# Optimization experiments

Hardware: AMD Instinct MI355X
Metric: run time of the kernel (lower is better)

Reference implementation:

```python
import jax, jax.numpy as jnp
import numpy as np

KH, KW = 3, 3
PAD = (1, 1, 1, 1)  # torch F.pad order: (W_left, W_right, H_top, H_bottom)
STRIDE = 1
B, CIN, COUT, H, W = 4, 32, 32, 128, 128


def setup_inputs() -> dict:
    key = jax.random.key(0)
    k1, k2, k3, k4 = jax.random.split(key, 4)
    f = jax.random.normal(k1, (B, CIN, H, W), jnp.float32)
    # orientation field components (cos/sin of a random angle field)
    theta = jax.random.uniform(k2, (B, CIN, H, W), jnp.float32, 0.0, 2.0 * np.pi)
    r0 = jnp.cos(theta)
    r1 = jnp.sin(theta)
    # learned conv weight (nn.Conv2d default uniform init, no bias)
    fan_in = CIN * KH * KW
    bound = 1.0 / np.sqrt(fan_in)
    w = jax.random.uniform(k3, (COUT, CIN, KH, KW), jnp.float32, -bound, bound)
    # frozen wr: (randn * pi * 100) / a with a = 100  ->  randn * pi
    wr = jax.random.normal(k4, (COUT, CIN, KH, KW), jnp.float32) * np.pi
    return {"f": f, "r0": r0, "r1": r1, "w": w, "wr": wr}


def _rot90(w):
    # torch: w.permute(0,1,2,4,3).flip([4]) on the (kh,kw) dims
    return jnp.flip(jnp.swapaxes(w, -1, -2), -1)


def _conv_single(f, r0, r1, w, wr):
    # f, r0, r1: (B, Cin, Hp, Wp);  w, wr: (Cout, Cin, KH, KW)
    Hp, Wp = f.shape[2], f.shape[3]
    he = Hp - PAD[0] - PAD[1]
    we = Wp - PAD[2] - PAD[3]
    s = STRIDE
    out = None
    for i in range(KH):
        for j in range(KW):
            fw = f[:, :, i:i + he:s, j:j + we:s]    # (B, Cin, h, w)
            r0w = r0[:, :, i:i + he:s, j:j + we:s]
            r1w = r1[:, :, i:i + he:s, j:j + we:s]
            c = jnp.cos(wr[:, :, i, j])[None, :, :, None, None]   # (1, Cout, Cin, 1, 1)
            sn = jnp.sin(wr[:, :, i, j])[None, :, :, None, None]
            # lambda_theta: relu of orientation-projected field, (B, Cout, Cin, h, w)
            lam = jax.nn.relu(c * r0w[:, None] + sn * r1w[:, None])
            term = jnp.einsum('bchw,oc,bochw->bohw', fw, w[:, :, i, j], lam)
            out = term if out is None else out + term
    return out  # (B, Cout, h, w)


def _forward(f, r0, r1, w, wr):
    pl, pr, pt, pb = PAD
    pad = ((0, 0), (0, 0), (pt, pb), (pl, pr))
    fp = jnp.pad(f, pad)
    r0p = jnp.pad(r0, pad)
    r1p = jnp.pad(r1, pad)
    orient = jnp.arange(4, dtype=f.dtype) * jnp.asarray(np.pi / 2, f.dtype)
    outs = []
    wk = w
    for o in range(4):
        if o > 0:
            wk = _rot90(wk)
        outs.append(_conv_single(fp, r0p, r1p, wk, wr + orient[o]))
    stacked = jnp.stack(outs, axis=2)              # (B, Cout, 4, h, w)
    idx = jnp.argmax(stacked, axis=2)              # (B, Cout, h, w)
    out = jnp.take_along_axis(stacked, idx[:, :, None], axis=2)[:, :, 0]
    out_r = orient[idx]                            # winning orientation angle
    return out, jnp.cos(out_r), jnp.sin(out_r)


def reference(f, r0, r1, w, wr):
    return _forward(f, r0, r1, w, wr)
```

## Files before the change

kernel.cpp:

```cpp
#include <hip/hip_runtime.h>


typedef float v2f __attribute__((ext_vector_type(2)));

#define B_    4
#define CIN_  32
#define COUT_ 32
#define H_    128
#define W_    128
#define HW_   (H_ * W_)
#define OUTSZ_ (B_ * COUT_ * H_ * W_)

__global__ __launch_bounds__(256)
void build_wtab(const float* __restrict__ w, const float* __restrict__ wr,
                float* __restrict__ tab)
{
    int idx = blockIdx.x * 256 + threadIdx.x;
    if (idx >= CIN_ * 9 * COUT_) return;
    int oc  = idx & 31;
    int t2  = idx >> 5;
    int tap = t2 % 9;
    int cc  = t2 / 9;
    int i = tap / 3, j = tap - i * 3;
    int base = (oc * CIN_ + cc) * 9;
    float w0 = w[base + i * 3 + j];
    float w1 = w[base + (2 - j) * 3 + i];
    float w2 = w[base + (2 - i) * 3 + (2 - j)];
    float w3 = w[base + j * 3 + (2 - i)];
    float S, C;
    sincosf(wr[base + i * 3 + j], &S, &C);
    float* dst = tab + (size_t)idx * 8;
    dst[0] = C;  dst[1] = S;
    dst[2] = w0; dst[3] = w1;
    dst[4] = w2; dst[5] = w3;
    dst[6] = 0.0f; dst[7] = 0.0f;
}

#define NC_    8
#define NG_    (CIN_ / NC_)
#define ROWF_  68
#define CLSTR_ (3 * ROWF_)
#define USED_  (NC_ * CLSTR_)
#define PLANE_ 1636
#define NBUF_  (3 * PLANE_)

struct WRow { float4 a0, a1, a2; float2 b0, b1, b2; };

#define LOAD_WROW(Wd) do {                                                  \
    const float* _wp = wanchor + soff;                                      \
    (Wd).a0 = *reinterpret_cast<const float4*>(_wp - 256);                  \
    (Wd).b0 = *reinterpret_cast<const float2*>(_wp - 252);                  \
    (Wd).a1 = *reinterpret_cast<const float4*>(_wp);                        \
    (Wd).b1 = *reinterpret_cast<const float2*>(_wp + 4);                    \
    (Wd).a2 = *reinterpret_cast<const float4*>(_wp + 256);                  \
    (Wd).b2 = *reinterpret_cast<const float2*>(_wp + 260);                  \
    soff += 768;                                                            \
    soff = (soff < 72960) ? soff : 72960;    \
    __builtin_amdgcn_sched_group_barrier(0x020, 6, 0);    \
} while (0)

#define CORE_TAP(W4, W2, JJ) do {                                           \
    v2f _C2  = {(W4).x, (W4).x};                                            \
    v2f _S2  = {(W4).y, (W4).y};                                            \
    v2f _w0  = {(W4).z, (W4).z};                                            \
    v2f _w1  = {(W4).w, (W4).w};                                            \
    v2f _w2  = {(W2).x, (W2).x};                                            \
    v2f _w3  = {(W2).y, (W2).y};                                            \
    _Pragma("unroll")                                                       \
    for (int _q = 0; _q < 2; ++_q) {                                        \
        v2f _f  = _fP[_q + (JJ)];                                           \
        v2f _r0 = _aP[_q + (JJ)];                                           \
        v2f _r1 = _bP[_q + (JJ)];                                           \
        v2f _m1 = _S2 * _r1;                                                \
        v2f _u  = __builtin_elementwise_fma(_C2, _r0, _m1);                 \
        v2f _m2 = _S2 * _r0;                                                \
        v2f _vv = __builtin_elementwise_fma(_C2, _r1, -_m2);                \
        v2f _g0 = __builtin_elementwise_max(_u,  (v2f)(0.0f));              \
        v2f _g1 = __builtin_elementwise_max(_vv, (v2f)(0.0f));              \
        v2f _t0 = _f * _g0;                                                 \
        v2f _t1 = _f * _g1;                                                 \
        v2f _t2 = __builtin_elementwise_fma(_f, -_u,  _t0);                 \
        v2f _t3 = __builtin_elementwise_fma(_f, -_vv, _t1);                 \
        acc[_q][0] = __builtin_elementwise_fma(_t0, _w0, acc[_q][0]);       \
        acc[_q][1] = __builtin_elementwise_fma(_t1, _w1, acc[_q][1]);       \
        acc[_q][2] = __builtin_elementwise_fma(_t2, _w2, acc[_q][2]);       \
        acc[_q][3] = __builtin_elementwise_fma(_t3, _w3, acc[_q][3]);       \
    }                                                                       \
} while (0)

#define COMPUTE_ROW(Wr, RB, CL, II) do {                                    \
    const float* _rb = (RB);                                                \
    const int _bi = (CL) * CLSTR_ + (II) * ROWF_ + (p << 1);                \
    float4 _fA = *reinterpret_cast<const float4*>(&_rb[_bi]);               \
    float4 _fB = *reinterpret_cast<const float4*>(&_rb[_bi + 4]);           \
    float4 _aA = *reinterpret_cast<const float4*>(&_rb[PLANE_ + _bi]);      \
    float4 _aB = *reinterpret_cast<const float4*>(&_rb[PLANE_ + _bi + 4]);  \
    float4 _bA = *reinterpret_cast<const float4*>(&_rb[2 * PLANE_ + _bi]);  \
    float4 _bB = *reinterpret_cast<const float4*>(&_rb[2 * PLANE_ + _bi + 4]);\
    v2f _fP[4] = {{_fA.x,_fA.y},{_fA.z,_fA.w},{_fB.x,_fB.y},{_fB.z,_fB.w}}; \
    v2f _aP[4] = {{_aA.x,_aA.y},{_aA.z,_aA.w},{_aB.x,_aB.y},{_aB.z,_aB.w}}; \
    v2f _bP[4] = {{_bA.x,_bA.y},{_bA.z,_bA.w},{_bB.x,_bB.y},{_bB.z,_bB.w}}; \
    CORE_TAP((Wr).a0, (Wr).b0, 0);                                          \
    CORE_TAP((Wr).a1, (Wr).b1, 1);                                          \
    CORE_TAP((Wr).a2, (Wr).b2, 2);                                          \
} while (0)

#define STEP(WLD, WUSE, RB, CL, II) do {                                    \
    LOAD_WROW(WLD);                                                         \
    COMPUTE_ROW(WUSE, RB, CL, II);                                          \
} while (0)

#define STAGE_LOAD(GI) do {                                                 \
    const int _gb = chanBase + (GI) * (NC_ * HW_);                          \
    const float* _fb = f  + _gb;                                            \
    const float* _ab = r0 + _gb;                                            \
    const float* _bb = r1 + _gb;                                            \
    _Pragma("unroll")                                                       \
    for (int _k = 0; _k < 3; ++_k) {                                        \
        tF[_k] = _fb[goff[_k]]; tA[_k] = _ab[goff[_k]]; tB[_k] = _bb[goff[_k]]; \
    }                                                                       \
    if (have3) { tF[3] = _fb[goff[3]]; tA[3] = _ab[goff[3]]; tB[3] = _bb[goff[3]]; } \
} while (0)

#define STAGE_WRITE(DST) do {                                               \
    float* _d = (DST);                                                      \
    _Pragma("unroll")                                                       \
    for (int _k = 0; _k < 3; ++_k) {                                        \
        _d[             sidx[_k]] = __uint_as_float(__float_as_uint(tF[_k]) & msk[_k]); \
        _d[PLANE_     + sidx[_k]] = __uint_as_float(__float_as_uint(tA[_k]) & msk[_k]); \
        _d[2 * PLANE_ + sidx[_k]] = __uint_as_float(__float_as_uint(tB[_k]) & msk[_k]); \
    }                                                                       \
    if (have3) {                                                            \
        _d[             sidx[3]] = __uint_as_float(__float_as_uint(tF[3]) & msk[3]); \
        _d[PLANE_     + sidx[3]] = __uint_as_float(__float_as_uint(tA[3]) & msk[3]); \
        _d[2 * PLANE_ + sidx[3]] = __uint_as_float(__float_as_uint(tB[3]) & msk[3]); \
    }                                                                       \
} while (0)

__global__ __launch_bounds__(512, 3)
void orient_conv_kernel(const float* __restrict__ f,
                        const float* __restrict__ r0,
                        const float* __restrict__ r1,
                        const float* __restrict__ tab,
                        float* __restrict__ out)
{
    __shared__ float sm[2 * NBUF_];

    const int tid   = threadIdx.x;
    const int oc    = tid & 31;
    const int pxg   = tid >> 5;
    const int p     = pxg << 1;
    const int obid  = blockIdx.x;
    const int bid   = (obid & 7) * ((B_ * H_ * 2) >> 3) + (obid >> 3);
    const int b     = bid >> 8;
    const int rem   = bid & 255;
    const int h     = rem >> 1;
    const int wbase = (rem & 1) << 6;

    int      goff[4], sidx[4];
    unsigned msk[4];
#pragma unroll
    for (int k = 0; k < 4; ++k) {
        int s = tid + (k << 9);
        if (s < USED_) {
            int cl  = s / CLSTR_;
            int r2  = s - cl * CLSTR_;
            int row = r2 / ROWF_;
            int q2  = r2 - row * ROWF_;
            int col = (q2 >> 1) + ((q2 & 1) << 5);
            int gh = h + row - 1;
            int gw = wbase + col - 1;
            bool ok = ((unsigned)gh < (unsigned)H_) & ((unsigned)gw < (unsigned)W_);
            goff[k] = ok ? (cl * HW_ + gh * W_ + gw) : 0;
            msk[k]  = ok ? 0xFFFFFFFFu : 0u;
            sidx[k] = s;
        } else { goff[k] = 0; msk[k] = 0u; sidx[k] = USED_; }
    }
    const bool have3 = (tid + 1536) < USED_;
    const int chanBase = b * (CIN_ * HW_);

    v2f acc[2][4];
#pragma unroll
    for (int q = 0; q < 2; ++q)
#pragma unroll
        for (int o = 0; o < 4; ++o) acc[q][o] = (v2f)(0.0f);

    const float* wanchor = tab + (size_t)((1 << 5) | oc) * 8;
    int soff = 0;
    WRow WA, WB;
    LOAD_WROW(WA);

    float tF[4], tA[4], tB[4];
    STAGE_LOAD(0);
    STAGE_WRITE(sm);
    STAGE_LOAD(1);
    __syncthreads();

#pragma unroll 1
    for (int g = 0; g < NG_; ++g) {
        const float* rb = sm + (g & 1) * NBUF_;

#pragma unroll 1
        for (int cl = 0; cl < NC_; cl += 2) {
            STEP(WB, WA, rb, cl,     0);
            STEP(WA, WB, rb, cl,     1);
            STEP(WB, WA, rb, cl,     2);
            STEP(WA, WB, rb, cl + 1, 0);
            STEP(WB, WA, rb, cl + 1, 1);
            STEP(WA, WB, rb, cl + 1, 2);
        }

        if (g + 1 < NG_) {
            float* wbuf = sm + ((g + 1) & 1) * NBUF_;
            STAGE_WRITE(wbuf);
            if (g + 2 < NG_) STAGE_LOAD(g + 2);
            __syncthreads();
        }
    }

    const float cosv[4] = {1.0f, -4.37113883e-08f, -1.0f, 1.19248806e-08f};
    const float sinv[4] = {0.0f, 1.0f, -8.74227766e-08f, -1.0f};
#pragma unroll
    for (int q = 0; q < 2; ++q) {
#pragma unroll
        for (int k = 0; k < 2; ++k) {
            int wcol = wbase + p + q + (k << 5);
            float a0 = acc[q][0][k], a1 = acc[q][1][k];
            float a2 = acc[q][2][k], a3 = acc[q][3][k];
            float best = a0; int bi = 0;
            if (a1 > best) { best = a1; bi = 1; }
            if (a2 > best) { best = a2; bi = 2; }
            if (a3 > best) { best = a3; bi = 3; }
            size_t o = ((size_t)(b * COUT_ + oc) * H_ + h) * W_ + wcol;
            out[o]              = best;
            out[o + OUTSZ_]     = cosv[bi];
            out[o + 2 * OUTSZ_] = sinv[bi];
        }
    }
}

extern "C" void kernel_launch(void* const* d_in, const int* in_sizes, int n_in,
                              void* d_out, int out_size, void* d_ws, size_t ws_size,
                              hipStream_t stream)
{
    const float* f  = (const float*)d_in[0];
    const float* r0 = (const float*)d_in[1];
    const float* r1 = (const float*)d_in[2];
    const float* w  = (const float*)d_in[3];
    const float* wr = (const float*)d_in[4];
    float* out = (float*)d_out;
    float* tab = (float*)d_ws;

    build_wtab<<<dim3(36), dim3(256), 0, stream>>>(w, wr, tab);
    orient_conv_kernel<<<dim3(B_ * H_ * 2), dim3(512), 0, stream>>>(
        f, r0, r1, tab, out);
}
```

Baseline: 267.7 us.

## Stage inputs via global_load_lds and software-pipeline LDS row reads

Replaces the register-staged global-to-LDS copy with direct global_load_lds async loads issued at the start of each channel group, then zeroes out-of-bounds halo entries in a fixup pass after waiting on vmcnt. It also double-buffers LDS row reads into registers (RA/RB) so the next row's ds_reads overlap the current row's math, and raises the occupancy hint in launch bounds from 3 to 4 blocks. The plane stride is changed so the wave-based LDS destination layout fits. This is meant to cut register pressure and staging latency, but it depends on the lane-to-address mapping of global_load_lds matching the thread-indexed layout, and the out-of-bounds lanes still issue loads from offset 0 that the fixup must overwrite.

```diff
diff --git a/kernel.cpp b/kernel.cpp
--- a/kernel.cpp
+++ b/kernel.cpp
@@ -41,10 +41,11 @@
 #define ROWF_  68
 #define CLSTR_ (3 * ROWF_)
 #define USED_  (NC_ * CLSTR_)
-#define PLANE_ 1636
+#define PLANE_ 1668
 #define NBUF_  (3 * PLANE_)
 
 struct WRow { float4 a0, a1, a2; float2 b0, b1, b2; };
+struct RRow { float4 f0, f1, a0, a1, b0, b1; };
 
 #define LOAD_WROW(Wd) do {                                                  \
     const float* _wp = wanchor + soff;                                      \
@@ -57,6 +58,17 @@
     soff += 768;                                                            \
     soff = (soff < 72960) ? soff : 72960;    \
     __builtin_amdgcn_sched_group_barrier(0x020, 6, 0);    \
+} while (0)
+
+#define RLOAD(Rd, RB_, CL, II) do {                                         \
+    const float* _rp = (RB_) + (CL) * CLSTR_ + (II) * ROWF_ + (p << 1);     \
+    (Rd).f0 = *reinterpret_cast<const float4*>(_rp);                        \
+    (Rd).f1 = *reinterpret_cast<const float4*>(_rp + 4);                    \
+    (Rd).a0 = *reinterpret_cast<const float4*>(_rp + PLANE_);               \
+    (Rd).a1 = *reinterpret_cast<const float4*>(_rp + PLANE_ + 4);           \
+    (Rd).b0 = *reinterpret_cast<const float4*>(_rp + 2 * PLANE_);           \
+    (Rd).b1 = *reinterpret_cast<const float4*>(_rp + 2 * PLANE_ + 4);       \
+    __builtin_amdgcn_sched_group_barrier(0x100, 6, 0);      \
 } while (0)
 
 #define CORE_TAP(W4, W2, JJ) do {                                           \
@@ -88,56 +100,67 @@
     }                                                                       \
 } while (0)
 
-#define COMPUTE_ROW(Wr, RB, CL, II) do {                                    \
-    const float* _rb = (RB);                                                \
-    const int _bi = (CL) * CLSTR_ + (II) * ROWF_ + (p << 1);                \
-    float4 _fA = *reinterpret_cast<const float4*>(&_rb[_bi]);               \
-    float4 _fB = *reinterpret_cast<const float4*>(&_rb[_bi + 4]);           \
-    float4 _aA = *reinterpret_cast<const float4*>(&_rb[PLANE_ + _bi]);      \
-    float4 _aB = *reinterpret_cast<const float4*>(&_rb[PLANE_ + _bi + 4]);  \
-    float4 _bA = *reinterpret_cast<const float4*>(&_rb[2 * PLANE_ + _bi]);  \
-    float4 _bB = *reinterpret_cast<const float4*>(&_rb[2 * PLANE_ + _bi + 4]);\
-    v2f _fP[4] = {{_fA.x,_fA.y},{_fA.z,_fA.w},{_fB.x,_fB.y},{_fB.z,_fB.w}}; \
-    v2f _aP[4] = {{_aA.x,_aA.y},{_aA.z,_aA.w},{_aB.x,_aB.y},{_aB.z,_aB.w}}; \
-    v2f _bP[4] = {{_bA.x,_bA.y},{_bA.z,_bA.w},{_bB.x,_bB.y},{_bB.z,_bB.w}}; \
+#define COMPUTE_R(Wr, Rs) do {                                              \
+    v2f _fP[4] = {{(Rs).f0.x,(Rs).f0.y},{(Rs).f0.z,(Rs).f0.w},              \
+                  {(Rs).f1.x,(Rs).f1.y},{(Rs).f1.z,(Rs).f1.w}};             \
+    v2f _aP[4] = {{(Rs).a0.x,(Rs).a0.y},{(Rs).a0.z,(Rs).a0.w},              \
+                  {(Rs).a1.x,(Rs).a1.y},{(Rs).a1.z,(Rs).a1.w}};             \
+    v2f _bP[4] = {{(Rs).b0.x,(Rs).b0.y},{(Rs).b0.z,(Rs).b0.w},              \
+                  {(Rs).b1.x,(Rs).b1.y},{(Rs).b1.z,(Rs).b1.w}};             \
     CORE_TAP((Wr).a0, (Wr).b0, 0);                                          \
     CORE_TAP((Wr).a1, (Wr).b1, 1);                                          \
     CORE_TAP((Wr).a2, (Wr).b2, 2);                                          \
 } while (0)
 
-#define STEP(WLD, WUSE, RB, CL, II) do {                                    \
+#define STEP_RW(WLD, WUSE, RLD, RUSE, RB_, CL, II) do {                     \
     LOAD_WROW(WLD);                                                         \
-    COMPUTE_ROW(WUSE, RB, CL, II);                                          \
-} while (0)
-
-#define STAGE_LOAD(GI) do {                                                 \
+    RLOAD(RLD, RB_, CL, II);                                                \
+    COMPUTE_R(WUSE, RUSE);                                                  \
+} while (0)
+
+#define STEP_LAST(WLD, WUSE, RUSE) do {                                     \
+    LOAD_WROW(WLD);                                                         \
+    COMPUTE_R(WUSE, RUSE);                                                  \
+} while (0)
+
+#define STAGE_GLL(GI, DSTBASE) do {                                         \
     const int _gb = chanBase + (GI) * (NC_ * HW_);                          \
-    const float* _fb = f  + _gb;                                            \
-    const float* _ab = r0 + _gb;                                            \
-    const float* _bb = r1 + _gb;                                            \
+    float* _db = (DSTBASE);                                                 \
     _Pragma("unroll")                                                       \
-    for (int _k = 0; _k < 3; ++_k) {                                        \
-        tF[_k] = _fb[goff[_k]]; tA[_k] = _ab[goff[_k]]; tB[_k] = _bb[goff[_k]]; \
+    for (int _k = 0; _k < 4; ++_k) {                                        \
+        if (_k < 3 || tid < 96) {                                           \
+            float* _l = _db + (_k << 9) + wvbase;                           \
+            const float* _gf = f  + _gb + goff[_k];                         \
+            const float* _ga = r0 + _gb + goff[_k];                         \
+            const float* _gr = r1 + _gb + goff[_k];                         \
+            __builtin_amdgcn_global_load_lds(                               \
+                (const __attribute__((address_space(1))) void*)_gf,         \
+                (__attribute__((address_space(3))) void*)(_l), 4, 0, 0);    \
+            __builtin_amdgcn_global_load_lds(                               \
+                (const __attribute__((address_space(1))) void*)_ga,         \
+                (__attribute__((address_space(3))) void*)(_l + PLANE_), 4, 0, 0); \
+            __builtin_amdgcn_global_load_lds(                               \
+                (const __attribute__((address_space(1))) void*)_gr,         \
+                (__attribute__((address_space(3))) void*)(_l + 2 * PLANE_), 4, 0, 0); \
+        }                                                                   \
     }                                                                       \
-    if (have3) { tF[3] = _fb[goff[3]]; tA[3] = _ab[goff[3]]; tB[3] = _bb[goff[3]]; } \
-} while (0)
-
-#define STAGE_WRITE(DST) do {                                               \
-    float* _d = (DST);                                                      \
+    __builtin_amdgcn_sched_group_barrier(0x010, 12, 0);                     \
+} while (0)
+
+#define FIXUP(DSTBASE) do {                                                 \
+    float* _db = (DSTBASE);                                                 \
     _Pragma("unroll")                                                       \
-    for (int _k = 0; _k < 3; ++_k) {                                        \
-        _d[             sidx[_k]] = __uint_as_float(__float_as_uint(tF[_k]) & msk[_k]); \
-        _d[PLANE_     + sidx[_k]] = __uint_as_float(__float_as_uint(tA[_k]) & msk[_k]); \
-        _d[2 * PLANE_ + sidx[_k]] = __uint_as_float(__float_as_uint(tB[_k]) & msk[_k]); \
+    for (int _k = 0; _k < 4; ++_k) {                                        \
+        int _s = tid + (_k << 9);                                           \
+        if (_s < USED_ && !((okbits >> _k) & 1)) {                          \
+            _db[_s] = 0.0f;                                                 \
+            _db[PLANE_ + _s] = 0.0f;                                        \
+            _db[2 * PLANE_ + _s] = 0.0f;                                    \
+        }                                                                   \
     }                                                                       \
-    if (have3) {                                                            \
-        _d[             sidx[3]] = __uint_as_float(__float_as_uint(tF[3]) & msk[3]); \
-        _d[PLANE_     + sidx[3]] = __uint_as_float(__float_as_uint(tA[3]) & msk[3]); \
-        _d[2 * PLANE_ + sidx[3]] = __uint_as_float(__float_as_uint(tB[3]) & msk[3]); \
-    }                                                                       \
-} while (0)
-
-__global__ __launch_bounds__(512, 3)
+} while (0)
+
+__global__ __launch_bounds__(512, 4)
 void orient_conv_kernel(const float* __restrict__ f,
                         const float* __restrict__ r0,
                         const float* __restrict__ r1,
@@ -146,10 +169,11 @@
 {
     __shared__ float sm[2 * NBUF_];
 
-    const int tid   = threadIdx.x;
-    const int oc    = tid & 31;
-    const int pxg   = tid >> 5;
-    const int p     = pxg << 1;
+    const int tid    = threadIdx.x;
+    const int oc     = tid & 31;
+    const int pxg    = tid >> 5;
+    const int p      = pxg << 1;
+    const int wvbase = tid & ~63;
     const int obid  = blockIdx.x;
     const int bid   = (obid & 7) * ((B_ * H_ * 2) >> 3) + (obid >> 3);
     const int b     = bid >> 8;
@@ -157,11 +181,12 @@
     const int h     = rem >> 1;
     const int wbase = (rem & 1) << 6;
 
-    int      goff[4], sidx[4];
-    unsigned msk[4];
+    int      goff[4];
+    unsigned okbits = 0;
 #pragma unroll
     for (int k = 0; k < 4; ++k) {
         int s = tid + (k << 9);
+        int ok = 0, go = 0;
         if (s < USED_) {
             int cl  = s / CLSTR_;
             int r2  = s - cl * CLSTR_;
@@ -170,13 +195,12 @@
             int col = (q2 >> 1) + ((q2 & 1) << 5);
             int gh = h + row - 1;
             int gw = wbase + col - 1;
-            bool ok = ((unsigned)gh < (unsigned)H_) & ((unsigned)gw < (unsigned)W_);
-            goff[k] = ok ? (cl * HW_ + gh * W_ + gw) : 0;
-            msk[k]  = ok ? 0xFFFFFFFFu : 0u;
-            sidx[k] = s;
-        } else { goff[k] = 0; msk[k] = 0u; sidx[k] = USED_; }
+            ok = ((unsigned)gh < (unsigned)H_) & ((unsigned)gw < (unsigned)W_);
+            go = ok ? (cl * HW_ + gh * W_ + gw) : 0;
+        }
+        goff[k] = go;
+        okbits |= (unsigned)ok << k;
     }
-    const bool have3 = (tid + 1536) < USED_;
     const int chanBase = b * (CIN_ * HW_);
 
     v2f acc[2][4];
@@ -188,32 +212,42 @@
     const float* wanchor = tab + (size_t)((1 << 5) | oc) * 8;
     int soff = 0;
     WRow WA, WB;
+    RRow RA, RB;
     LOAD_WROW(WA);
 
-    float tF[4], tA[4], tB[4];
-    STAGE_LOAD(0);
-    STAGE_WRITE(sm);
-    STAGE_LOAD(1);
+    STAGE_GLL(0, sm);
+    asm volatile("s_waitcnt vmcnt(0)" ::: "memory");
+    FIXUP(sm);
     __syncthreads();
 
 #pragma unroll 1
     for (int g = 0; g < NG_; ++g) {
-        const float* rb = sm + (g & 1) * NBUF_;
+        float* cur = sm + (g & 1) * NBUF_;
+        float* nxt = sm + ((g + 1) & 1) * NBUF_;
+
+        if (g + 1 < NG_) STAGE_GLL(g + 1, nxt);
+
+        RLOAD(RA, cur, 0, 0);
 
 #pragma unroll 1
-        for (int cl = 0; cl < NC_; cl += 2) {
-            STEP(WB, WA, rb, cl,     0);
-            STEP(WA, WB, rb, cl,     1);
-            STEP(WB, WA, rb, cl,     2);
-            STEP(WA, WB, rb, cl + 1, 0);
-            STEP(WB, WA, rb, cl + 1, 1);
-            STEP(WA, WB, rb, cl + 1, 2);
-        }
+        for (int cl = 0; cl < NC_ - 2; cl += 2) {
+            STEP_RW(WB, WA, RB, RA, cur, cl,     1);
+            STEP_RW(WA, WB, RA, RB, cur, cl,     2);
+            STEP_RW(WB, WA, RB, RA, cur, cl + 1, 0);
+            STEP_RW(WA, WB, RA, RB, cur, cl + 1, 1);
+            STEP_RW(WB, WA, RB, RA, cur, cl + 1, 2);
+            STEP_RW(WA, WB, RA, RB, cur, cl + 2, 0);
+        }
+        STEP_RW(WB, WA, RB, RA, cur, 6, 1);
+        STEP_RW(WA, WB, RA, RB, cur, 6, 2);
+        STEP_RW(WB, WA, RB, RA, cur, 7, 0);
+        STEP_RW(WA, WB, RA, RB, cur, 7, 1);
+        STEP_RW(WB, WA, RB, RA, cur, 7, 2);
+        STEP_LAST(WA, WB, RB);
 
         if (g + 1 < NG_) {
-            float* wbuf = sm + ((g + 1) & 1) * NBUF_;
-            STAGE_WRITE(wbuf);
-            if (g + 2 < NG_) STAGE_LOAD(g + 2);
+            asm volatile("s_waitcnt vmcnt(0)" ::: "memory");
+            FIXUP(nxt);
             __syncthreads();
         }
     }
```

New measurement: 638.8 us. 139% more time.
